# Kernel tuning notes

Measured on AMD Instinct MI355X. Metric: run time of the kernel, lower is better.

The kernel has to match this reference:

```python
import jax, jax.numpy as jnp
import numpy as np

N_NODES = 30000
N_EDGES = 480000
IN_FEAT = 256
OUT_FEAT = 256
N_RELS = 8
N_HEADS = 4
HEAD_DIM = OUT_FEAT // N_HEADS
LEAKY_SLOPE = 0.2


def setup_inputs() -> dict:
    key = jax.random.key(0)
    ks = jax.random.split(key, 8)
    inputs = jax.random.normal(ks[0], (N_NODES, IN_FEAT), dtype=jnp.float32)
    conv_weights = jax.random.normal(ks[1], (N_RELS, N_HEADS, IN_FEAT, HEAD_DIM), dtype=jnp.float32) * (1.0 / np.sqrt(IN_FEAT))
    attn_l = jax.random.normal(ks[2], (N_RELS, N_HEADS, HEAD_DIM), dtype=jnp.float32) * 0.1
    attn_r = jax.random.normal(ks[3], (N_RELS, N_HEADS, HEAD_DIM), dtype=jnp.float32) * 0.1
    h_bias = jax.random.normal(ks[4], (OUT_FEAT,), dtype=jnp.float32) * 0.02
    edge_src = jax.random.randint(ks[5], (N_EDGES,), 0, N_NODES, dtype=jnp.int32)
    edge_dst = jax.random.randint(ks[6], (N_EDGES,), 0, N_NODES, dtype=jnp.int32)
    edge_type = jax.random.randint(ks[7], (N_EDGES,), 0, N_RELS, dtype=jnp.int32)
    return {"inputs": inputs, "conv_weights": conv_weights, "attn_l": attn_l,
            "attn_r": attn_r, "h_bias": h_bias, "edge_src": edge_src,
            "edge_dst": edge_dst, "edge_type": edge_type}


def reference(inputs, conv_weights, attn_l, attn_r, h_bias, edge_src, edge_dst, edge_type):
    # Per-relation dense transform of all node features: [R, N, H, D]
    feat_all = jnp.einsum('ni,rhid->rnhd', inputs, conv_weights)
    # Gather transformed source/destination features per edge: [E, H, D]
    feat_src_e = feat_all[edge_type, edge_src]
    feat_dst_e = feat_all[edge_type, edge_dst]
    # Per-edge attention logits (relation-specific attn vectors): [E, H]
    el = jnp.sum(feat_src_e * attn_l[edge_type], axis=-1)
    er = jnp.sum(feat_dst_e * attn_r[edge_type], axis=-1)
    e = jax.nn.leaky_relu(el + er, negative_slope=LEAKY_SLOPE)
    # Segment softmax over incoming edges of each destination node
    m = jax.ops.segment_max(e, edge_dst, num_segments=N_NODES)  # [N, H]
    ex = jnp.exp(e - m[edge_dst])
    denom = jax.ops.segment_sum(ex, edge_dst, num_segments=N_NODES)  # [N, H]
    alpha = ex / denom[edge_dst]  # [E, H]
    # Attention-weighted aggregation of transformed source features
    h = jax.ops.segment_sum(alpha[..., None] * feat_src_e, edge_dst, num_segments=N_NODES)  # [N, H, D]
    h = h.reshape(N_NODES, OUT_FEAT) + h_bias
    # activation=None, self_loop=False, dropout=0.0 (eval) -> identity
    return h
```

## Files before the change

### kernel.cpp

```cpp
#include <hip/hip_runtime.h>
#include <hip/hip_bf16.h>

#define N_NODES 30000
#define NPAD    30080
#define N_EDGES 480000
#define N_RELS  8
#define NB_SCAN 118

typedef short bf16x8 __attribute__((ext_vector_type(8)));
typedef float f32x4  __attribute__((ext_vector_type(4)));

__device__ __forceinline__ unsigned short f2bf(float f) {
    unsigned u = __float_as_uint(f);
    u += 0x7fffu + ((u >> 16) & 1u);
    return (unsigned short)(u >> 16);
}
__device__ __forceinline__ float bf2f(unsigned short h) {
    return __uint_as_float(((unsigned)h) << 16);
}
__device__ __forceinline__ ushort2 pk2bf(float a, float b) {
    __hip_bfloat162 t = __float22bfloat162_rn(float2{a, b});
    union { __hip_bfloat162 h; ushort2 u; } cv; cv.h = t; return cv.u;
}

__device__ __forceinline__ void load_lds16(const void* g, void* l) {
    __builtin_amdgcn_global_load_lds(
        (const __attribute__((address_space(1))) unsigned int*)g,
        (__attribute__((address_space(3))) unsigned int*)l,
        16, 0, 0);
}

__global__ void prep_kernel(const float* __restrict__ x, unsigned short* __restrict__ xbf,
                            const float* __restrict__ cw, unsigned short* __restrict__ wt,
                            const int* __restrict__ edst, int* __restrict__ counts) {
    int b = blockIdx.x;
    if (b < 3760) {
        int t = b * 256 + threadIdx.x;
        int base = t * 8;
        int n = base >> 8;
        unsigned short h[8];
        if (n < N_NODES) {
            float4 a = *(const float4*)(x + base);
            float4 c = *(const float4*)(x + base + 4);
            h[0]=f2bf(a.x); h[1]=f2bf(a.y); h[2]=f2bf(a.z); h[3]=f2bf(a.w);
            h[4]=f2bf(c.x); h[5]=f2bf(c.y); h[6]=f2bf(c.z); h[7]=f2bf(c.w);
        } else {
            #pragma unroll
            for (int i = 0; i < 8; ++i) h[i] = 0;
        }
        uint4 o;
        o.x = (unsigned)h[0] | ((unsigned)h[1] << 16);
        o.y = (unsigned)h[2] | ((unsigned)h[3] << 16);
        o.z = (unsigned)h[4] | ((unsigned)h[5] << 16);
        o.w = (unsigned)h[6] | ((unsigned)h[7] << 16);
        *(uint4*)(xbf + base) = o;
    } else if (b < 5808) {
        int o = (b - 3760) * 256 + threadIdx.x;
        int i = o & 255;
        int c = (o >> 8) & 255;
        int r = o >> 16;
        float v = cw[(((size_t)r * 4 + (c >> 6)) * 256 + i) * 64 + (c & 63)];
        wt[o] = f2bf(v);
    } else {
        int e = (b - 5808) * 256 + threadIdx.x;
        if (e < N_EDGES) atomicAdd(&counts[edst[e]], 1);
    }
}

__global__ void scan1_kernel(const int* __restrict__ counts, int* __restrict__ locexcl,
                             int* __restrict__ bsum) {
    __shared__ int sm[256];
    int tid = threadIdx.x;
    int idx = blockIdx.x * 256 + tid;
    int v = (idx < N_NODES) ? counts[idx] : 0;
    sm[tid] = v;
    __syncthreads();
    for (int o = 1; o < 256; o <<= 1) {
        int t = (tid >= o) ? sm[tid - o] : 0;
        __syncthreads();
        sm[tid] += t;
        __syncthreads();
    }
    int incl = sm[tid];
    if (idx < N_NODES) locexcl[idx] = incl - v;
    if (tid == 255) bsum[blockIdx.x] = incl;
}

__global__ void scan2_kernel(const int* __restrict__ bsum, int* __restrict__ bpre) {
    __shared__ int sm[128];
    int tid = threadIdx.x;
    int v = (tid < NB_SCAN) ? bsum[tid] : 0;
    sm[tid] = v;
    __syncthreads();
    for (int o = 1; o < 128; o <<= 1) {
        int t = (tid >= o) ? sm[tid - o] : 0;
        __syncthreads();
        sm[tid] += t;
        __syncthreads();
    }
    if (tid < NB_SCAN) bpre[tid] = sm[tid] - v;
}

__global__ void scan3_kernel(const int* __restrict__ locexcl, const int* __restrict__ bpre,
                             int* __restrict__ offsets, int* __restrict__ cursor) {
    int idx = blockIdx.x * 256 + threadIdx.x;
    if (idx < N_NODES) {
        int o = bpre[blockIdx.x] + locexcl[idx];
        offsets[idx] = o;
        cursor[idx]  = o;
    }
    if (idx == 0) offsets[N_NODES] = N_EDGES;
}

__global__ __launch_bounds__(256) void gemm_kernel(
    const unsigned short* __restrict__ xbf,
    const unsigned short* __restrict__ wt,
    const float* __restrict__ attn_l,
    const float* __restrict__ attn_r,
    unsigned short* __restrict__ feat,
    float* __restrict__ projl,
    float* __restrict__ projr)
{
    __shared__ __align__(16) unsigned char smem[32768];

    const int tid  = threadIdx.x;
    const int lane = tid & 63;
    const int w    = tid >> 6;
    const int wm   = w >> 1;
    const int wn   = w & 1;
    const int quad = lane >> 4;
    const int l15  = lane & 15;

    const int bid  = blockIdx.x;
    const int work = (bid & 7) * 470 + (bid >> 3);
    const int mt   = work >> 4;
    const int r    = (work >> 1) & 7;
    const int nt   = work & 1;
    const int mbase = mt * 128;
    const int nbase = nt * 128;

    const unsigned short* Asrc = xbf + (size_t)mbase * 256;
    const unsigned short* Bsrc = wt + ((size_t)r * 256 + nbase) * 256;

    f32x4 acc[4][4] = {};

    const int srow = w * 16 + (lane >> 2);
    const int c0   = lane & 3;

    for (int k0 = 0; k0 < 256; k0 += 32) {
        #pragma unroll
        for (int n = 0; n < 2; ++n) {
            int row = n * 64 + srow;
            int c   = c0 ^ ((row >> 1) & 3);
            load_lds16(Asrc + (size_t)row * 256 + k0 + c * 8, smem + (n * 256 + w * 64) * 16);
        }
        #pragma unroll
        for (int n = 0; n < 2; ++n) {
            int row = n * 64 + srow;
            int c   = c0 ^ ((row >> 1) & 3);
            load_lds16(Bsrc + (size_t)row * 256 + k0 + c * 8, smem + 8192 + (n * 256 + w * 64) * 16);
        }
        __syncthreads();

        bf16x8 xf[4], wf[4];
        #pragma unroll
        for (int j = 0; j < 4; ++j) {
            int row = wm * 64 + j * 16 + l15;
            int cc  = quad ^ ((row >> 1) & 3);
            xf[j] = *(const bf16x8*)(smem + row * 64 + cc * 16);
        }
        #pragma unroll
        for (int i = 0; i < 4; ++i) {
            int row = wn * 64 + i * 16 + l15;
            int cc  = quad ^ ((row >> 1) & 3);
            wf[i] = *(const bf16x8*)(smem + 8192 + row * 64 + cc * 16);
        }

        #pragma unroll
        for (int i = 0; i < 4; ++i)
            #pragma unroll
            for (int j = 0; j < 4; ++j)
                acc[i][j] = __builtin_amdgcn_mfma_f32_16x16x32_bf16(wf[i], xf[j], acc[i][j], 0, 0, 0);
        __syncthreads();
    }

    #pragma unroll
    for (int j = 0; j < 4; ++j) {
        int node = mbase + wm * 64 + j * 16 + l15;
        size_t rowb = ((size_t)r * NPAD + node) * 256 + nbase + wn * 64;
        #pragma unroll
        for (int i = 0; i < 4; ++i) {
            ushort2 lo = pk2bf(acc[i][j][0], acc[i][j][1]);
            ushort2 hi = pk2bf(acc[i][j][2], acc[i][j][3]);
            ushort4 v;
            v.x = lo.x; v.y = lo.y; v.z = hi.x; v.w = hi.y;
            *(ushort4*)(feat + rowb + i * 16 + quad * 4) = v;
        }
    }

    const int head = nt * 2 + wn;
    float alv[4][4], arv[4][4];
    #pragma unroll
    for (int i = 0; i < 4; ++i)
        #pragma unroll
        for (int e = 0; e < 4; ++e) {
            int c = i * 16 + quad * 4 + e;
            alv[i][e] = attn_l[((size_t)r * 4 + head) * 64 + c];
            arv[i][e] = attn_r[((size_t)r * 4 + head) * 64 + c];
        }
    float* bufL = (float*)smem + w * 1024;
    float* bufR = (float*)(smem + 16384) + w * 1024;
    #pragma unroll
    for (int j = 0; j < 4; ++j) {
        float s1 = 0.f, s2 = 0.f;
        #pragma unroll
        for (int i = 0; i < 4; ++i)
            #pragma unroll
            for (int e = 0; e < 4; ++e) {
                s1 += acc[i][j][e] * alv[i][e];
                s2 += acc[i][j][e] * arv[i][e];
            }
        int node = j * 16 + l15;
        bufL[node * 5 + quad] = s1;
        bufR[node * 5 + quad] = s2;
    }
    float sL = 0.f, sR = 0.f;
    #pragma unroll
    for (int q = 0; q < 4; ++q) {
        sL += bufL[lane * 5 + q];
        sR += bufR[lane * 5 + q];
    }
    int g = mbase + wm * 64 + lane;
    projl[((size_t)r * NPAD + g) * 4 + head] = sL;
    projr[((size_t)r * NPAD + g) * 4 + head] = sR;
}

__global__ void logits_scatter_kernel(
    const int* __restrict__ esrc, const int* __restrict__ edst, const int* __restrict__ etyp,
    const float* __restrict__ projl, const float* __restrict__ projr,
    int* __restrict__ cursor, int* __restrict__ srcoff, float* __restrict__ exw)
{
    int e = blockIdx.x * 256 + threadIdx.x;
    if (e >= N_EDGES) return;
    int s = esrc[e], d = edst[e], t = etyp[e];
    float4 pl = ((const float4*)projl)[(size_t)t * NPAD + s];
    float4 pr = ((const float4*)projr)[(size_t)t * NPAD + d];
    float4 o;
    float v;
    v = pl.x + pr.x; v = v > 0.f ? v : 0.2f * v; o.x = __expf(v);
    v = pl.y + pr.y; v = v > 0.f ? v : 0.2f * v; o.y = __expf(v);
    v = pl.z + pr.z; v = v > 0.f ? v : 0.2f * v; o.z = __expf(v);
    v = pl.w + pr.w; v = v > 0.f ? v : 0.2f * v; o.w = __expf(v);
    int p = atomicAdd(&cursor[d], 1);
    srcoff[p] = t * NPAD + s;
    ((float4*)exw)[p] = o;
}

__global__ __launch_bounds__(256) void aggregate_kernel(
    const int* __restrict__ offsets, const int* __restrict__ srcoff,
    const float* __restrict__ exw, const unsigned short* __restrict__ feat,
    const float* __restrict__ bias, float* __restrict__ out)
{
    __shared__ float sm[2][64][5];
    int wid  = threadIdx.x >> 6;
    int slot = wid >> 1;
    int half = wid & 1;
    int v = blockIdx.x * 2 + slot;
    int lane = threadIdx.x & 63;
    int head = lane >> 4;
    int s0 = offsets[v], s1 = offsets[v + 1];
    int mid = s0 + ((s1 - s0 + 1) >> 1);
    int lo = half ? mid : s0;
    int hi = half ? s1  : mid;
    float a0 = 0.f, a1 = 0.f, a2 = 0.f, a3 = 0.f, den = 0.f;
    int i = lo;
    for (; i + 8 <= hi; i += 8) {
        int o[8]; float ee[8]; ushort4 ff[8];
        #pragma unroll
        for (int u = 0; u < 8; ++u) { o[u] = srcoff[i + u]; ee[u] = exw[(size_t)(i + u) * 4 + head]; }
        #pragma unroll
        for (int u = 0; u < 8; ++u) ff[u] = *(const ushort4*)(feat + (size_t)o[u] * 256 + lane * 4);
        #pragma unroll
        for (int u = 0; u < 8; ++u) {
            den += ee[u];
            a0 += ee[u] * bf2f(ff[u].x);
            a1 += ee[u] * bf2f(ff[u].y);
            a2 += ee[u] * bf2f(ff[u].z);
            a3 += ee[u] * bf2f(ff[u].w);
        }
    }
    for (; i + 4 <= hi; i += 4) {
        int o[4]; float ee[4]; ushort4 ff[4];
        #pragma unroll
        for (int u = 0; u < 4; ++u) { o[u] = srcoff[i + u]; ee[u] = exw[(size_t)(i + u) * 4 + head]; }
        #pragma unroll
        for (int u = 0; u < 4; ++u) ff[u] = *(const ushort4*)(feat + (size_t)o[u] * 256 + lane * 4);
        #pragma unroll
        for (int u = 0; u < 4; ++u) {
            den += ee[u];
            a0 += ee[u] * bf2f(ff[u].x);
            a1 += ee[u] * bf2f(ff[u].y);
            a2 += ee[u] * bf2f(ff[u].z);
            a3 += ee[u] * bf2f(ff[u].w);
        }
    }
    for (; i + 2 <= hi; i += 2) {
        int o[2]; float ee[2]; ushort4 ff[2];
        #pragma unroll
        for (int u = 0; u < 2; ++u) { o[u] = srcoff[i + u]; ee[u] = exw[(size_t)(i + u) * 4 + head]; }
        #pragma unroll
        for (int u = 0; u < 2; ++u) ff[u] = *(const ushort4*)(feat + (size_t)o[u] * 256 + lane * 4);
        #pragma unroll
        for (int u = 0; u < 2; ++u) {
            den += ee[u];
            a0 += ee[u] * bf2f(ff[u].x);
            a1 += ee[u] * bf2f(ff[u].y);
            a2 += ee[u] * bf2f(ff[u].z);
            a3 += ee[u] * bf2f(ff[u].w);
        }
    }
    if (i < hi) {
        int o0 = srcoff[i];
        float e0 = exw[(size_t)i * 4 + head];
        ushort4 f0 = *(const ushort4*)(feat + (size_t)o0 * 256 + lane * 4);
        den += e0;
        a0 += e0 * bf2f(f0.x);
        a1 += e0 * bf2f(f0.y);
        a2 += e0 * bf2f(f0.z);
        a3 += e0 * bf2f(f0.w);
    }
    if (half) {
        sm[slot][lane][0] = a0; sm[slot][lane][1] = a1;
        sm[slot][lane][2] = a2; sm[slot][lane][3] = a3;
        sm[slot][lane][4] = den;
    }
    __syncthreads();
    if (!half) {
        a0 += sm[slot][lane][0]; a1 += sm[slot][lane][1];
        a2 += sm[slot][lane][2]; a3 += sm[slot][lane][3];
        den += sm[slot][lane][4];
        float inv = den > 0.f ? 1.f / den : 0.f;
        float4 o;
        o.x = a0 * inv + bias[lane * 4 + 0];
        o.y = a1 * inv + bias[lane * 4 + 1];
        o.z = a2 * inv + bias[lane * 4 + 2];
        o.w = a3 * inv + bias[lane * 4 + 3];
        ((float4*)out)[(size_t)v * 64 + lane] = o;
    }
}

extern "C" void kernel_launch(void* const* d_in, const int* in_sizes, int n_in,
                              void* d_out, int out_size, void* d_ws, size_t ws_size,
                              hipStream_t stream) {
    const float* x    = (const float*)d_in[0];
    const float* cw   = (const float*)d_in[1];
    const float* al   = (const float*)d_in[2];
    const float* ar   = (const float*)d_in[3];
    const float* bias = (const float*)d_in[4];
    const int* esrc   = (const int*)d_in[5];
    const int* edst   = (const int*)d_in[6];
    const int* etyp   = (const int*)d_in[7];
    float* out        = (float*)d_out;

    char* ws = (char*)d_ws;
    size_t off = 0;
    auto alloc = [&](size_t bytes) { size_t o = off; off += (bytes + 255) & ~(size_t)255; return o; };

    unsigned short* xbf  = (unsigned short*)(ws + alloc((size_t)NPAD * 256 * 2));
    unsigned short* wt   = (unsigned short*)(ws + alloc((size_t)N_RELS * 256 * 256 * 2));
    unsigned short* feat = (unsigned short*)(ws + alloc((size_t)N_RELS * NPAD * 256 * 2));
    float* projl = (float*)(ws + alloc((size_t)N_RELS * NPAD * 4 * 4));
    float* projr = (float*)(ws + alloc((size_t)N_RELS * NPAD * 4 * 4));
    float* exw   = (float*)(ws + alloc((size_t)N_EDGES * 4 * 4));
    int* srcoff  = (int*)(ws + alloc((size_t)N_EDGES * 4));
    int* counts  = (int*)(ws + alloc((size_t)N_NODES * 4));
    int* offsets = (int*)(ws + alloc((size_t)(N_NODES + 1) * 4));
    int* cursor  = (int*)(ws + alloc((size_t)N_NODES * 4));
    int* locexcl = (int*)(ws + alloc((size_t)N_NODES * 4));
    int* bsum    = (int*)(ws + alloc((size_t)NB_SCAN * 4));
    int* bpre    = (int*)(ws + alloc((size_t)NB_SCAN * 4));

    hipMemsetAsync(counts, 0, (size_t)N_NODES * 4, stream);

    prep_kernel<<<7683, 256, 0, stream>>>(x, xbf, cw, wt, edst, counts);
    scan1_kernel<<<NB_SCAN, 256, 0, stream>>>(counts, locexcl, bsum);
    scan2_kernel<<<1, 128, 0, stream>>>(bsum, bpre);
    scan3_kernel<<<NB_SCAN, 256, 0, stream>>>(locexcl, bpre, offsets, cursor);
    gemm_kernel<<<3760, 256, 0, stream>>>(xbf, wt, al, ar, feat, projl, projr);
    logits_scatter_kernel<<<1875, 256, 0, stream>>>(esrc, edst, etyp, projl, projr,
                                                    cursor, srcoff, exw);
    aggregate_kernel<<<15000, 256, 0, stream>>>(offsets, srcoff, exw, feat, bias, out);
}
```

Measured before the change: 258.2 us.

## Double-buffer LDS tiles in the per-relation GEMM K-loop

Converts the bf16 MFMA GEMM K-loop to a two-stage LDS ping-pong. The next K-slice of A and B is issued into the alternate buffer before the MFMAs on the current slice, and the loop is fully unrolled with precomputed swizzled offsets. This is meant to hide global-to-LDS load latency behind MFMA work and drop one barrier per iteration. It doubles the LDS footprint to 32 KB, which may reduce occupancy and needs the shared buffer to be sized for it.

```diff
diff --git a/kernel.cpp b/kernel.cpp
--- a/kernel.cpp
+++ b/kernel.cpp
@@ -147,33 +147,46 @@
     const int srow = w * 16 + (lane >> 2);
     const int c0   = lane & 3;
 
-    for (int k0 = 0; k0 < 256; k0 += 32) {
-        #pragma unroll
-        for (int n = 0; n < 2; ++n) {
-            int row = n * 64 + srow;
-            int c   = c0 ^ ((row >> 1) & 3);
-            load_lds16(Asrc + (size_t)row * 256 + k0 + c * 8, smem + (n * 256 + w * 64) * 16);
-        }
-        #pragma unroll
-        for (int n = 0; n < 2; ++n) {
-            int row = n * 64 + srow;
-            int c   = c0 ^ ((row >> 1) & 3);
-            load_lds16(Bsrc + (size_t)row * 256 + k0 + c * 8, smem + 8192 + (n * 256 + w * 64) * 16);
-        }
-        __syncthreads();
+    const int row0 = srow,      cs0 = c0 ^ ((row0 >> 1) & 3);
+    const int row1 = 64 + srow, cs1 = c0 ^ ((row1 >> 1) & 3);
+    const size_t aoff0 = (size_t)row0 * 256 + cs0 * 8;
+    const size_t aoff1 = (size_t)row1 * 256 + cs1 * 8;
+    const int ldst0 = (w * 64) * 16;
+    const int ldst1 = (256 + w * 64) * 16;
+
+    load_lds16(Asrc + aoff0, smem + ldst0);
+    load_lds16(Asrc + aoff1, smem + ldst1);
+    load_lds16(Bsrc + aoff0, smem + 16384 + ldst0);
+    load_lds16(Bsrc + aoff1, smem + 16384 + ldst1);
+    __syncthreads();
+
+    #pragma unroll
+    for (int it = 0; it < 8; ++it) {
+        const int cur = it & 1;
+        const unsigned abase = cur * 8192;
+        const unsigned bbase = 16384 + cur * 8192;
+
+        if (it < 7) {
+            const int nxt = cur ^ 1;
+            const size_t k0 = (size_t)(it + 1) * 32;
+            load_lds16(Asrc + k0 + aoff0, smem + nxt * 8192 + ldst0);
+            load_lds16(Asrc + k0 + aoff1, smem + nxt * 8192 + ldst1);
+            load_lds16(Bsrc + k0 + aoff0, smem + 16384 + nxt * 8192 + ldst0);
+            load_lds16(Bsrc + k0 + aoff1, smem + 16384 + nxt * 8192 + ldst1);
+        }
 
         bf16x8 xf[4], wf[4];
         #pragma unroll
         for (int j = 0; j < 4; ++j) {
             int row = wm * 64 + j * 16 + l15;
             int cc  = quad ^ ((row >> 1) & 3);
-            xf[j] = *(const bf16x8*)(smem + row * 64 + cc * 16);
+            xf[j] = *(const bf16x8*)(smem + abase + row * 64 + cc * 16);
         }
         #pragma unroll
         for (int i = 0; i < 4; ++i) {
             int row = wn * 64 + i * 16 + l15;
             int cc  = quad ^ ((row >> 1) & 3);
-            wf[i] = *(const bf16x8*)(smem + 8192 + row * 64 + cc * 16);
+            wf[i] = *(const bf16x8*)(smem + bbase + row * 64 + cc * 16);
         }
 
         #pragma unroll
@@ -181,6 +194,7 @@
             #pragma unroll
             for (int j = 0; j < 4; ++j)
                 acc[i][j] = __builtin_amdgcn_mfma_f32_16x16x32_bf16(wf[i], xf[j], acc[i][j], 0, 0, 0);
+
         __syncthreads();
     }
 
```

After: 265.0 us. +2.6%, slower.
